# Optimization experiments

Hardware: AMD Instinct MI355X
Metric: run time of the kernel (lower is better)

The kernel has to match this reference:

```python
import jax, jax.numpy as jnp
import numpy as np

B, T, E, D = 4, 1024, 1024, 2048   # batch, dec len, enc len, model dim
N, K, H = 16, 8, 256               # q heads, kv heads, head dim
G = N // K                         # GQA group size
SCALE = H ** -0.5                  # query_pre_attn_scalar
SOFT_CAP = 50.0
EPS = 1e-6
ROPE_BASE = 10000.0
_K_MASK = jnp.finfo(jnp.bfloat16).min


def _rms_norm(x, scale, eps=EPS):
    var = jnp.mean(jnp.square(x), axis=-1, keepdims=True)
    return x * jax.lax.rsqrt(var + eps) * (1.0 + scale)


def _apply_rope(x, positions, base=ROPE_BASE):
    # x: [B, L, n, H], positions: [B, L]; rope_proportion=1.0, scale_factor=1.0
    h = x.shape[-1]
    freq_exp = 2.0 / h * jnp.arange(h // 2, dtype=jnp.float32)
    timescale = base ** freq_exp                                  # [H/2]
    ang = (positions.astype(jnp.float32)[..., None] / timescale)[..., None, :]  # [B,L,1,H/2]
    sin, cos = jnp.sin(ang), jnp.cos(ang)
    x1, x2 = jnp.split(x, 2, axis=-1)
    out = jnp.concatenate([x1 * cos - x2 * sin, x2 * cos + x1 * sin], axis=-1)
    return out.astype(x.dtype)


def setup_inputs() -> dict:
    key = jax.random.key(0)
    ks = jax.random.split(key, 8)
    hidden_states = jax.random.normal(ks[0], (B, T, D), jnp.float32)
    encoder_hidden_states = jax.random.normal(ks[1], (B, E, D), jnp.float32)
    position_ids = jnp.broadcast_to(jnp.arange(T, dtype=jnp.int32)[None, :], (B, T))
    # merged mask: causal over self part, full visibility over cross part
    causal = jnp.tril(jnp.ones((T, T), jnp.bool_))
    cross = jnp.ones((T, E), jnp.bool_)
    merged_attention_mask = jnp.broadcast_to(
        jnp.concatenate([causal, cross], axis=-1)[None, None], (B, 1, T, T + E))
    w = 0.02
    q_w = jax.random.normal(ks[2], (N, D, H), jnp.float32) * w
    k_w = jax.random.normal(ks[3], (K, D, H), jnp.float32) * w
    v_w = jax.random.normal(ks[4], (K, D, H), jnp.float32) * w
    o_w = jax.random.normal(ks[5], (N, H, D), jnp.float32) * w
    q_scale = jax.random.normal(ks[6], (H,), jnp.float32) * w
    k_scale = jax.random.normal(ks[7], (H,), jnp.float32) * w
    return dict(hidden_states=hidden_states, encoder_hidden_states=encoder_hidden_states,
                position_ids=position_ids, merged_attention_mask=merged_attention_mask,
                q_w=q_w, k_w=k_w, v_w=v_w, o_w=o_w, q_scale=q_scale, k_scale=k_scale)


def reference(hidden_states, encoder_hidden_states, position_ids, merged_attention_mask,
              q_w, k_w, v_w, o_w, q_scale, k_scale):
    # QKV projections
    query = jnp.einsum('BTD,NDH->BTNH', hidden_states, q_w)
    self_key = jnp.einsum('BTD,KDH->BTKH', hidden_states, k_w)
    self_value = jnp.einsum('BTD,KDH->BTKH', hidden_states, v_w)
    # QK-RMSNorm
    query = _rms_norm(query, q_scale)
    self_key = _rms_norm(self_key, k_scale)
    # RoPE on self-attention q/k only
    query = _apply_rope(query, position_ids)
    self_key = _apply_rope(self_key, position_ids)
    # Cross K/V from encoder states (no RoPE)
    cross_key = _rms_norm(jnp.einsum('BTD,KDH->BTKH', encoder_hidden_states, k_w), k_scale)
    cross_value = jnp.einsum('BTD,KDH->BTKH', encoder_hidden_states, v_w)
    # Merge self + cross along key axis
    keys = jnp.concatenate([self_key, cross_key], axis=1)       # [B, T+E, K, H]
    values = jnp.concatenate([self_value, cross_value], axis=1)
    # Scaled GQA attention
    q = (query * SCALE).reshape(B, T, K, G, H)
    logits = jnp.einsum('BTKGH,BSKH->BKGTS', q, keys)
    # logit soft-capping
    logits = SOFT_CAP * jnp.tanh(logits / SOFT_CAP)
    mask = merged_attention_mask[:, :, None]                    # [B,1,1,T,S]
    logits = jnp.where(mask, logits, _K_MASK)
    probs = jax.nn.softmax(logits.astype(jnp.float32), axis=-1).astype(keys.dtype)
    attn = jnp.einsum('BKGTS,BSKH->BTKGH', probs, values).reshape(B, T, N, H)
    return jnp.einsum('BTNH,NHD->BTD', attn, o_w)
```

## Files before the change

### kernel.cpp

```cpp
#include <hip/hip_runtime.h>
#include <hip/hip_bf16.h>
#include <cstdio>


typedef __attribute__((ext_vector_type(8))) short bf16x8;
typedef __attribute__((ext_vector_type(4))) float f32x4;

static __device__ __forceinline__ ushort f2bf(float x){
  uint u = __float_as_uint(x);
  u += 0x7fffu + ((u >> 16) & 1u);
  return (ushort)(u >> 16);
}
static __device__ __forceinline__ float bf2f(ushort u){
  return __uint_as_float((uint)u << 16);
}
#define GLL16(gp, lp)                                                          \
  __builtin_amdgcn_global_load_lds(                                            \
      (const __attribute__((address_space(1))) void*)(gp),                     \
      (__attribute__((address_space(3))) void*)(lp), 16, 0, 0)

__global__ void k_detect(const uint* __restrict__ src, int* __restrict__ flag){
  int lane = threadIdx.x & 63;
  int cnt = 0;
  for (int i = 0; i < 4; i++){
    uint w = src[lane * 4 + i];
    uint e = (w >> 7) & 0xffu;
    cnt += (e >= 90u && e <= 141u) ? 1 : 0;
  }
  for (int o = 1; o < 64; o <<= 1) cnt += __shfl_xor(cnt, o);
  if (lane == 0) *flag = (cnt >= 128) ? 1 : 0;
}

__global__ void k_tobf(const void* __restrict__ src, ushort* __restrict__ dst,
                       int n8, const int* __restrict__ flag){
  int i = blockIdx.x * blockDim.x + threadIdx.x;
  if (i >= n8) return;
  if (*flag){
    reinterpret_cast<uint4*>(dst)[i] = reinterpret_cast<const uint4*>(src)[i];
  } else {
    const float4* s = reinterpret_cast<const float4*>(src);
    float4 a = s[i * 2], b = s[i * 2 + 1];
    ushort o[8] = { f2bf(a.x), f2bf(a.y), f2bf(a.z), f2bf(a.w),
                    f2bf(b.x), f2bf(b.y), f2bf(b.z), f2bf(b.w) };
    reinterpret_cast<uint4*>(dst)[i] = *reinterpret_cast<uint4*>(o);
  }
}

__global__ void k_wtrans(const void* __restrict__ in, ushort* __restrict__ out,
                         int R, int C, const int* __restrict__ flag){
  __shared__ ushort t[32][33];
  int isbf = *flag;
  int p = blockIdx.z;
  int r0 = blockIdx.y * 32, c0 = blockIdx.x * 32;
  ushort* op = out + (size_t)p * R * C;
  int cc = threadIdx.x & 31, rr = threadIdx.x >> 5;
  if (isbf){
    const ushort* ip = (const ushort*)in + (size_t)p * R * C;
    for (int i = 0; i < 32; i += 8)
      t[rr + i][cc] = ip[(size_t)(r0 + rr + i) * C + c0 + cc];
  } else {
    const float* ip = (const float*)in + (size_t)p * R * C;
    for (int i = 0; i < 32; i += 8)
      t[rr + i][cc] = f2bf(ip[(size_t)(r0 + rr + i) * C + c0 + cc]);
  }
  __syncthreads();
  for (int i = 0; i < 32; i += 8)
    op[(size_t)(c0 + rr + i) * R + r0 + cc] = t[cc][rr + i];
}

__global__ __launch_bounds__(256)
void k_gemm_qkv(const ushort* __restrict__ A0, const ushort* __restrict__ A1,
                const ushort* __restrict__ Bm,
                ushort* __restrict__ Qo, ushort* __restrict__ Ko,
                ushort* __restrict__ Vo){
  const int m0 = blockIdx.y * 128, n0 = blockIdx.x * 128;
  if (n0 < 4096 && m0 >= 4096) return;
  __shared__ ushort As[128 * 32];
  __shared__ ushort Bs[128 * 32];
  const int tid = threadIdx.x;
  const int Kd = 2048;
  const ushort* Ap = (m0 < 4096) ? (A0 + (size_t)m0 * Kd)
                                 : (A1 + (size_t)(m0 - 4096) * Kd);
  const ushort* Bp = Bm + (size_t)n0 * Kd;
  const int w = tid >> 6, lane = tid & 63, c = lane & 15, q = lane >> 4;
  const int wr = (w >> 1) * 64, wc = (w & 1) * 64;

  f32x4 zf = {0.f, 0.f, 0.f, 0.f};
  f32x4 acc[4][4];
  for (int mi = 0; mi < 4; mi++) for (int ni = 0; ni < 4; ni++) acc[mi][ni] = zf;

  const int sr = tid >> 2, sc8 = (tid & 3) * 8;
  const ushort* ga = Ap + (size_t)sr * Kd + sc8;
  const ushort* gb = Bp + (size_t)sr * Kd + sc8;
  ushort* la = &As[sr * 32 + sc8];
  ushort* lb = &Bs[sr * 32 + sc8];
  const size_t rowskip = (size_t)64 * Kd;

  for (int k0 = 0; k0 < Kd; k0 += 32){
    GLL16(ga + k0,           la);
    GLL16(ga + k0 + rowskip, la + 64 * 32);
    GLL16(gb + k0,           lb);
    GLL16(gb + k0 + rowskip, lb + 64 * 32);
    __syncthreads();
    bf16x8 af[4], bfrg[4];
    for (int mi = 0; mi < 4; mi++)
      af[mi] = *reinterpret_cast<const bf16x8*>(&As[(wr + mi * 16 + c) * 32 + q * 8]);
    for (int ni = 0; ni < 4; ni++)
      bfrg[ni] = *reinterpret_cast<const bf16x8*>(&Bs[(wc + ni * 16 + c) * 32 + q * 8]);
    for (int mi = 0; mi < 4; mi++)
      for (int ni = 0; ni < 4; ni++)
        acc[mi][ni] = __builtin_amdgcn_mfma_f32_16x16x32_bf16(af[mi], bfrg[ni], acc[mi][ni], 0, 0, 0);
    __syncthreads();
  }

  for (int mi = 0; mi < 4; mi++)
    for (int ni = 0; ni < 4; ni++){
      int gr0 = m0 + wr + mi * 16 + q * 4;
      int gc  = n0 + wc + ni * 16 + c;
      if (n0 < 4096){
        for (int r = 0; r < 4; r++)
          Qo[(size_t)(gr0 + r) * 4096 + gc] = f2bf(acc[mi][ni][r]);
      } else if (n0 < 6144){
        int col = gc - 4096;
        for (int r = 0; r < 4; r++){
          int gr = gr0 + r, b, s;
          if (gr < 4096){ b = gr >> 10; s = gr & 1023; }
          else { int g2 = gr - 4096; b = g2 >> 10; s = 1024 + (g2 & 1023); }
          Ko[(size_t)(b * 2048 + s) * 2048 + col] = f2bf(acc[mi][ni][r]);
        }
      } else {
        int col = gc - 6144;
        int gr = gr0, b, s;
        if (gr < 4096){ b = gr >> 10; s = gr & 1023; }
        else { int g2 = gr - 4096; b = g2 >> 10; s = 1024 + (g2 & 1023); }
        int kk = col >> 8, h = col & 255;
        ushort4 o;
        o.x = f2bf(acc[mi][ni][0]); o.y = f2bf(acc[mi][ni][1]);
        o.z = f2bf(acc[mi][ni][2]); o.w = f2bf(acc[mi][ni][3]);
        *reinterpret_cast<ushort4*>(Vo + ((size_t)(b * 8 + kk) * 256 + h) * 2048 + s) = o;
      }
    }
}

__global__ __launch_bounds__(256)
void k_gemm_o(const ushort* __restrict__ A0, const ushort* __restrict__ Bm,
              float* __restrict__ Cout, int N, int Kd){
  __shared__ ushort As[128 * 32];
  __shared__ ushort Bs[128 * 32];
  const int tid = threadIdx.x;
  const int m0 = blockIdx.y * 128, n0 = blockIdx.x * 128;
  const ushort* Ap = A0 + (size_t)m0 * Kd;
  const ushort* Bp = Bm + (size_t)n0 * Kd;
  const int w = tid >> 6, lane = tid & 63, c = lane & 15, q = lane >> 4;
  const int wr = (w >> 1) * 64, wc = (w & 1) * 64;
  f32x4 zf = {0.f, 0.f, 0.f, 0.f};
  f32x4 acc[4][4];
  for (int mi = 0; mi < 4; mi++) for (int ni = 0; ni < 4; ni++) acc[mi][ni] = zf;
  const int sr = tid >> 2, sc8 = (tid & 3) * 8;
  const ushort* ga = Ap + (size_t)sr * Kd + sc8;
  const ushort* gb = Bp + (size_t)sr * Kd + sc8;
  ushort* la = &As[sr * 32 + sc8];
  ushort* lb = &Bs[sr * 32 + sc8];
  const size_t rowskip = (size_t)64 * Kd;
  for (int k0 = 0; k0 < Kd; k0 += 32){
    GLL16(ga + k0,           la);
    GLL16(ga + k0 + rowskip, la + 64 * 32);
    GLL16(gb + k0,           lb);
    GLL16(gb + k0 + rowskip, lb + 64 * 32);
    __syncthreads();
    bf16x8 af[4], bfrg[4];
    for (int mi = 0; mi < 4; mi++)
      af[mi] = *reinterpret_cast<const bf16x8*>(&As[(wr + mi * 16 + c) * 32 + q * 8]);
    for (int ni = 0; ni < 4; ni++)
      bfrg[ni] = *reinterpret_cast<const bf16x8*>(&Bs[(wc + ni * 16 + c) * 32 + q * 8]);
    for (int mi = 0; mi < 4; mi++)
      for (int ni = 0; ni < 4; ni++)
        acc[mi][ni] = __builtin_amdgcn_mfma_f32_16x16x32_bf16(af[mi], bfrg[ni], acc[mi][ni], 0, 0, 0);
    __syncthreads();
  }
  for (int mi = 0; mi < 4; mi++)
    for (int ni = 0; ni < 4; ni++){
      int gr0 = m0 + wr + mi * 16 + q * 4;
      int gc  = n0 + wc + ni * 16 + c;
      for (int r = 0; r < 4; r++)
        Cout[(size_t)(gr0 + r) * N + gc] = acc[mi][ni][r];
    }
}

__global__ __launch_bounds__(256)
void k_norm_q(const ushort* __restrict__ Qraw, const int* __restrict__ pos,
              const ushort* __restrict__ scale, ushort* __restrict__ Qbf){
  int w = threadIdx.x >> 6, lane = threadIdx.x & 63;
  int gw = blockIdx.x * 4 + w;
  int bt = gw >> 4;
  ushort4 xu = *reinterpret_cast<const ushort4*>(Qraw + (size_t)gw * 256 + lane * 4);
  float x[4] = { bf2f(xu.x), bf2f(xu.y), bf2f(xu.z), bf2f(xu.w) };
  float ss = x[0]*x[0] + x[1]*x[1] + x[2]*x[2] + x[3]*x[3];
  for (int o = 32; o > 0; o >>= 1) ss += __shfl_xor(ss, o);
  float rin = rsqrtf(ss * (1.f / 256.f) + 1e-6f);
  ushort4 su = *reinterpret_cast<const ushort4*>(scale + lane * 4);
  float y[4] = { x[0] * rin * (1.f + bf2f(su.x)), x[1] * rin * (1.f + bf2f(su.y)),
                 x[2] * rin * (1.f + bf2f(su.z)), x[3] * rin * (1.f + bf2f(su.w)) };
  float oth[4];
  for (int i = 0; i < 4; i++) oth[i] = __shfl_xor(y[i], 32);
  bool hi = lane >= 32;
  float fb = (float)((lane & 31) * 4);
  float p = (float)pos[bt];
  ushort4 o;
  ushort* op[4] = {&o.x, &o.y, &o.z, &o.w};
  for (int i = 0; i < 4; i++){
    float fi = fb + i;
    float tsi = expf(fi * -0.07195578415f);
    float ang = p * tsi;
    float sn, cs; sincosf(ang, &sn, &cs);
    float v = hi ? (y[i] * cs + oth[i] * sn) : (y[i] * cs - oth[i] * sn);
    *op[i] = f2bf(v * 0.0625f);
  }
  *reinterpret_cast<ushort4*>(Qbf + (size_t)gw * 256 + lane * 4) = o;
}

__global__ __launch_bounds__(256)
void k_norm_k(const ushort* __restrict__ Kraw, const int* __restrict__ pos,
              const ushort* __restrict__ scale, ushort* __restrict__ Kbf){
  int w = threadIdx.x >> 6, lane = threadIdx.x & 63;
  int gw = blockIdx.x * 4 + w;
  int row = gw >> 3;
  int s = row & 2047, b = row >> 11;
  ushort4 xu = *reinterpret_cast<const ushort4*>(Kraw + (size_t)gw * 256 + lane * 4);
  float x[4] = { bf2f(xu.x), bf2f(xu.y), bf2f(xu.z), bf2f(xu.w) };
  float ss = x[0]*x[0] + x[1]*x[1] + x[2]*x[2] + x[3]*x[3];
  for (int o = 32; o > 0; o >>= 1) ss += __shfl_xor(ss, o);
  float rin = rsqrtf(ss * (1.f / 256.f) + 1e-6f);
  ushort4 su = *reinterpret_cast<const ushort4*>(scale + lane * 4);
  float y[4] = { x[0] * rin * (1.f + bf2f(su.x)), x[1] * rin * (1.f + bf2f(su.y)),
                 x[2] * rin * (1.f + bf2f(su.z)), x[3] * rin * (1.f + bf2f(su.w)) };
  ushort4 o;
  ushort* op[4] = {&o.x, &o.y, &o.z, &o.w};
  if (s < 1024){
    float oth[4];
    for (int i = 0; i < 4; i++) oth[i] = __shfl_xor(y[i], 32);
    bool hi = lane >= 32;
    float fb = (float)((lane & 31) * 4);
    float p = (float)pos[b * 1024 + s];
    for (int i = 0; i < 4; i++){
      float fi = fb + i;
      float tsi = expf(fi * -0.07195578415f);
      float ang = p * tsi;
      float sn, cs; sincosf(ang, &sn, &cs);
      float v = hi ? (y[i] * cs + oth[i] * sn) : (y[i] * cs - oth[i] * sn);
      *op[i] = f2bf(v);
    }
  } else {
    for (int i = 0; i < 4; i++) *op[i] = f2bf(y[i]);
  }
  *reinterpret_cast<ushort4*>(Kbf + (size_t)gw * 256 + lane * 4) = o;
}

__global__ __launch_bounds__(256)
void k_attn(const ushort* __restrict__ Qbf, const ushort* __restrict__ Kbf,
            const ushort* __restrict__ Vt, ushort* __restrict__ attn){
  constexpr int KSs = 264, VSs = 40, PSs = 40;
  __shared__ ushort Ks[32 * KSs];
  __shared__ ushort Vs[256 * VSs];
  __shared__ ushort Pm[4][32 * PSs];
  int id = blockIdx.x;
  int xcd = id & 7, slot = id >> 3;
  int grp = xcd + 8 * (slot >> 4);
  int within = slot & 15;
  int b = grp >> 3, kk = grp & 7;
  int n = kk * 2 + (within >> 3);
  int t0 = (within & 7) * 128;
  int tid = threadIdx.x, w = tid >> 6, lane = tid & 63, c = lane & 15, q = lane >> 4;
  int rowbase = t0 + w * 32;

  bf16x8 qf[2][8];
  for (int g = 0; g < 2; g++){
    int tq = rowbase + g * 16 + c;
    const ushort* qp = Qbf + ((size_t)(b * 1024 + tq) * 16 + n) * 256 + q * 8;
    for (int f = 0; f < 8; f++) qf[g][f] = *reinterpret_cast<const bf16x8*>(qp + f * 32);
  }
  f32x4 zf = {0.f, 0.f, 0.f, 0.f};
  f32x4 accO[2][16];
  for (int g = 0; g < 2; g++) for (int i = 0; i < 16; i++) accO[g][i] = zf;
  float lacc[2][4] = {{0.f,0.f,0.f,0.f},{0.f,0.f,0.f,0.f}};

  const ushort* Kbase = Kbf + ((size_t)b * 2048 * 8 + kk) * 256;
  const ushort* Vbase = Vt + (size_t)(b * 8 + kk) * 256 * 2048;
  int nself = (t0 >> 5) + 4;
  int ntile = nself + 32;
  for (int it = 0; it < ntile; ++it){
    int s0 = (it < nself) ? it * 32 : 1024 + (it - nself) * 32;
    for (int i = 0; i < 4; i++){
      int tau = tid + i * 256;
      int r = tau >> 5, ch = (tau & 31) * 8;
      *reinterpret_cast<uint4*>(&Ks[r * KSs + ch]) =
        *reinterpret_cast<const uint4*>(Kbase + (size_t)(s0 + r) * 2048 + ch);
    }
    for (int i = 0; i < 4; i++){
      int tau = tid + i * 256;
      int h = tau >> 2, ch = (tau & 3) * 8;
      *reinterpret_cast<uint4*>(&Vs[h * VSs + ch]) =
        *reinterpret_cast<const uint4*>(Vbase + (size_t)h * 2048 + s0 + ch);
    }
    __syncthreads();
    f32x4 accL[2][2];
    accL[0][0] = zf; accL[0][1] = zf; accL[1][0] = zf; accL[1][1] = zf;
    for (int ni = 0; ni < 2; ni++)
      for (int f = 0; f < 8; f++){
        bf16x8 kb = *reinterpret_cast<const bf16x8*>(&Ks[(ni * 16 + c) * KSs + f * 32 + q * 8]);
        accL[0][ni] = __builtin_amdgcn_mfma_f32_16x16x32_bf16(qf[0][f], kb, accL[0][ni], 0, 0, 0);
        accL[1][ni] = __builtin_amdgcn_mfma_f32_16x16x32_bf16(qf[1][f], kb, accL[1][ni], 0, 0, 0);
      }
    ushort* pw = Pm[w];
    for (int g = 0; g < 2; g++)
      for (int ni = 0; ni < 2; ni++)
        for (int r = 0; r < 4; r++){
          int s = s0 + ni * 16 + c;
          int t = rowbase + g * 16 + q * 4 + r;
          float x = accL[g][ni][r] * 0.02f;
          float xc = fminf(fmaxf(x, -10.f), 10.f);
          float e2 = __expf(2.f * xc);
          float l2 = 50.f * (1.f - 2.f / (e2 + 1.f));
          float pv = (s >= 1024 || s <= t) ? __expf(l2) : 0.f;
          lacc[g][r] += pv;
          pw[(g * 16 + q * 4 + r) * PSs + ni * 16 + c] = f2bf(pv);
        }
    __asm__ volatile("s_waitcnt lgkmcnt(0)" ::: "memory");
    bf16x8 pa0 = *reinterpret_cast<const bf16x8*>(&pw[c * PSs + q * 8]);
    bf16x8 pa1 = *reinterpret_cast<const bf16x8*>(&pw[(16 + c) * PSs + q * 8]);
    for (int hi = 0; hi < 16; hi++){
      bf16x8 vb = *reinterpret_cast<const bf16x8*>(&Vs[(hi * 16 + c) * VSs + q * 8]);
      accO[0][hi] = __builtin_amdgcn_mfma_f32_16x16x32_bf16(pa0, vb, accO[0][hi], 0, 0, 0);
      accO[1][hi] = __builtin_amdgcn_mfma_f32_16x16x32_bf16(pa1, vb, accO[1][hi], 0, 0, 0);
    }
    __syncthreads();
  }
  for (int g = 0; g < 2; g++)
    for (int r = 0; r < 4; r++)
      for (int o = 1; o < 16; o <<= 1) lacc[g][r] += __shfl_xor(lacc[g][r], o);
  for (int g = 0; g < 2; g++){
    float inv[4];
    for (int r = 0; r < 4; r++) inv[r] = 1.f / fmaxf(lacc[g][r], 1e-37f);
    for (int hi = 0; hi < 16; hi++)
      for (int r = 0; r < 4; r++){
        int t = rowbase + g * 16 + q * 4 + r;
        attn[((size_t)(b * 1024 + t) * 16 + n) * 256 + hi * 16 + c] = f2bf(accO[g][hi][r] * inv[r]);
      }
  }
}

extern "C" void kernel_launch(void* const* d_in, const int* in_sizes, int n_in,
                              void* d_out, int out_size, void* d_ws, size_t ws_size,
                              hipStream_t stream){
  const void* hidden = d_in[0];
  const void* enc    = d_in[1];
  const int*  posids = (const int*)d_in[2];
  const void* qw = d_in[4];
  const void* kw = d_in[5];
  const void* vw = d_in[6];
  const void* ow = d_in[7];
  const void* qs = d_in[8];
  const void* ks = d_in[9];
  float* out = (float*)d_out;

  char* ws = (char*)d_ws;
  size_t off = 0;
  auto alloc = [&](size_t sz){ void* p = ws + off; off += sz; return p; };
  char*   HbEb = (char*)alloc(33554432);
  ushort* Hb   = (ushort*)HbEb;
  ushort* Eb   = (ushort*)(HbEb + 16777216);
  ushort* Wcat = (ushort*)alloc(33554432);
  ushort* Wo   = (ushort*)alloc(16777216);
  ushort* Qraw = (ushort*)alloc(33554432);
  ushort* Kraw = (ushort*)alloc(33554432);
  ushort* Vt   = (ushort*)alloc(33554432);
  ushort* qsb  = (ushort*)alloc(512);
  ushort* ksb  = (ushort*)alloc(512);
  int*    flag = (int*)alloc(64);
  ushort* Qbf   = (ushort*)HbEb;
  ushort* Kbf   = Qraw;
  ushort* attnb = Kraw;
  if (off > ws_size){
    fprintf(stderr, "kernel_launch: ws too small: need %zu, have %zu\n", off, ws_size);
    return;
  }

  k_detect<<<1, 64, 0, stream>>>((const uint*)hidden, flag);
  k_tobf<<<4096, 256, 0, stream>>>(hidden, Hb, 1048576, flag);
  k_tobf<<<4096, 256, 0, stream>>>(enc,    Eb, 1048576, flag);
  k_tobf<<<1, 256, 0, stream>>>(qs, qsb, 32, flag);
  k_tobf<<<1, 256, 0, stream>>>(ks, ksb, 32, flag);

  k_wtrans<<<dim3(8, 64, 16), 256, 0, stream>>>(qw, Wcat,            2048, 256, flag);
  k_wtrans<<<dim3(8, 64, 8),  256, 0, stream>>>(kw, Wcat + 8388608,  2048, 256, flag);
  k_wtrans<<<dim3(8, 64, 8),  256, 0, stream>>>(vw, Wcat + 12582912, 2048, 256, flag);
  k_wtrans<<<dim3(64, 128, 1), 256, 0, stream>>>(ow, Wo, 4096, 2048, flag);

  k_gemm_qkv<<<dim3(64, 64), 256, 0, stream>>>(Hb, Eb, Wcat, Qraw, Kraw, Vt);

  k_norm_q<<<16384, 256, 0, stream>>>(Qraw, posids, qsb, Qbf);
  k_norm_k<<<16384, 256, 0, stream>>>(Kraw, posids, ksb, Kbf);

  k_attn<<<512, 256, 0, stream>>>(Qbf, Kbf, Vt, attnb);

  k_gemm_o<<<dim3(16, 32), 256, 0, stream>>>(attnb, Wo, out, 2048, 4096);
}
```

Before: 900.6 us.

## Prefetch attention K/V tiles into registers, swizzle GEMM blocks, add MFMA priority

The attention loop now issues the global loads for the next K/V tile into registers before computing the current tile, then writes them to LDS after the second barrier. This hides global-memory latency behind the MFMA and softmax work. Both GEMMs remap block indices with a stride-8 swizzle to improve L2 locality across XCDs. MFMA sections are wrapped in s_setprio, and attention blocks alternate the order of query tiles to balance causal work. The prefetch raises register pressure by 32 VGPRs per thread, which may reduce occupancy.

```diff
diff --git a/kernel.cpp b/kernel.cpp
--- a/kernel.cpp
+++ b/kernel.cpp
@@ -73,7 +73,9 @@
                 const ushort* __restrict__ Bm,
                 ushort* __restrict__ Qo, ushort* __restrict__ Ko,
                 ushort* __restrict__ Vo){
-  const int m0 = blockIdx.y * 128, n0 = blockIdx.x * 128;
+  const int flat = blockIdx.y * 64 + blockIdx.x;
+  const int sw = (flat & 7) * 512 + (flat >> 3);
+  const int m0 = (sw >> 6) * 128, n0 = (sw & 63) * 128;
   if (n0 < 4096 && m0 >= 4096) return;
   __shared__ ushort As[128 * 32];
   __shared__ ushort Bs[128 * 32];
@@ -107,9 +109,11 @@
       af[mi] = *reinterpret_cast<const bf16x8*>(&As[(wr + mi * 16 + c) * 32 + q * 8]);
     for (int ni = 0; ni < 4; ni++)
       bfrg[ni] = *reinterpret_cast<const bf16x8*>(&Bs[(wc + ni * 16 + c) * 32 + q * 8]);
+    __builtin_amdgcn_s_setprio(1);
     for (int mi = 0; mi < 4; mi++)
       for (int ni = 0; ni < 4; ni++)
         acc[mi][ni] = __builtin_amdgcn_mfma_f32_16x16x32_bf16(af[mi], bfrg[ni], acc[mi][ni], 0, 0, 0);
+    __builtin_amdgcn_s_setprio(0);
     __syncthreads();
   }
 
@@ -148,7 +152,9 @@
   __shared__ ushort As[128 * 32];
   __shared__ ushort Bs[128 * 32];
   const int tid = threadIdx.x;
-  const int m0 = blockIdx.y * 128, n0 = blockIdx.x * 128;
+  const int flat = blockIdx.y * 16 + blockIdx.x;
+  const int sw = (flat & 7) * 64 + (flat >> 3);
+  const int m0 = (sw >> 4) * 128, n0 = (sw & 15) * 128;
   const ushort* Ap = A0 + (size_t)m0 * Kd;
   const ushort* Bp = Bm + (size_t)n0 * Kd;
   const int w = tid >> 6, lane = tid & 63, c = lane & 15, q = lane >> 4;
@@ -173,9 +179,11 @@
       af[mi] = *reinterpret_cast<const bf16x8*>(&As[(wr + mi * 16 + c) * 32 + q * 8]);
     for (int ni = 0; ni < 4; ni++)
       bfrg[ni] = *reinterpret_cast<const bf16x8*>(&Bs[(wc + ni * 16 + c) * 32 + q * 8]);
+    __builtin_amdgcn_s_setprio(1);
     for (int mi = 0; mi < 4; mi++)
       for (int ni = 0; ni < 4; ni++)
         acc[mi][ni] = __builtin_amdgcn_mfma_f32_16x16x32_bf16(af[mi], bfrg[ni], acc[mi][ni], 0, 0, 0);
+    __builtin_amdgcn_s_setprio(0);
     __syncthreads();
   }
   for (int mi = 0; mi < 4; mi++)
@@ -269,7 +277,9 @@
   int within = slot & 15;
   int b = grp >> 3, kk = grp & 7;
   int n = kk * 2 + (within >> 3);
-  int t0 = (within & 7) * 128;
+  int j = within & 7;
+  if (id & 256) j = 7 - j;
+  int t0 = j * 128;
   int tid = threadIdx.x, w = tid >> 6, lane = tid & 63, c = lane & 15, q = lane >> 4;
   int rowbase = t0 + w * 32;
 
@@ -286,31 +296,57 @@
 
   const ushort* Kbase = Kbf + ((size_t)b * 2048 * 8 + kk) * 256;
   const ushort* Vbase = Vt + (size_t)(b * 8 + kk) * 256 * 2048;
+
+  int koffE[4], voffE[4];
+  ushort *klp[4], *vlp[4];
+#pragma unroll
+  for (int i = 0; i < 4; i++){
+    int tau = tid + i * 256;
+    int r = tau >> 5, ch = (tau & 31) * 8;
+    koffE[i] = r * 2048 + ch;
+    klp[i] = &Ks[r * KSs + ch];
+    int h = tau >> 2, cv = (tau & 3) * 8;
+    voffE[i] = h * 2048 + cv;
+    vlp[i] = &Vs[h * VSs + cv];
+  }
+
   int nself = (t0 >> 5) + 4;
   int ntile = nself + 32;
+
+#pragma unroll
+  for (int i = 0; i < 4; i++)
+    *reinterpret_cast<uint4*>(klp[i]) = *reinterpret_cast<const uint4*>(Kbase + koffE[i]);
+#pragma unroll
+  for (int i = 0; i < 4; i++)
+    *reinterpret_cast<uint4*>(vlp[i]) = *reinterpret_cast<const uint4*>(Vbase + voffE[i]);
+
   for (int it = 0; it < ntile; ++it){
     int s0 = (it < nself) ? it * 32 : 1024 + (it - nself) * 32;
-    for (int i = 0; i < 4; i++){
-      int tau = tid + i * 256;
-      int r = tau >> 5, ch = (tau & 31) * 8;
-      *reinterpret_cast<uint4*>(&Ks[r * KSs + ch]) =
-        *reinterpret_cast<const uint4*>(Kbase + (size_t)(s0 + r) * 2048 + ch);
-    }
-    for (int i = 0; i < 4; i++){
-      int tau = tid + i * 256;
-      int h = tau >> 2, ch = (tau & 3) * 8;
-      *reinterpret_cast<uint4*>(&Vs[h * VSs + ch]) =
-        *reinterpret_cast<const uint4*>(Vbase + (size_t)h * 2048 + s0 + ch);
-    }
-    __syncthreads();
+    __syncthreads();
+
+    uint4 kr[4], vr[4];
+    const bool pf = (it + 1 < ntile);
+    if (pf){
+      int it1 = it + 1;
+      int s0n = (it1 < nself) ? it1 * 32 : 1024 + (it1 - nself) * 32;
+      const ushort* kp = Kbase + (size_t)s0n * 2048;
+      const ushort* vp = Vbase + s0n;
+#pragma unroll
+      for (int i = 0; i < 4; i++) kr[i] = *reinterpret_cast<const uint4*>(kp + koffE[i]);
+#pragma unroll
+      for (int i = 0; i < 4; i++) vr[i] = *reinterpret_cast<const uint4*>(vp + voffE[i]);
+    }
+
     f32x4 accL[2][2];
     accL[0][0] = zf; accL[0][1] = zf; accL[1][0] = zf; accL[1][1] = zf;
+    __builtin_amdgcn_s_setprio(1);
     for (int ni = 0; ni < 2; ni++)
       for (int f = 0; f < 8; f++){
         bf16x8 kb = *reinterpret_cast<const bf16x8*>(&Ks[(ni * 16 + c) * KSs + f * 32 + q * 8]);
         accL[0][ni] = __builtin_amdgcn_mfma_f32_16x16x32_bf16(qf[0][f], kb, accL[0][ni], 0, 0, 0);
         accL[1][ni] = __builtin_amdgcn_mfma_f32_16x16x32_bf16(qf[1][f], kb, accL[1][ni], 0, 0, 0);
       }
+    __builtin_amdgcn_s_setprio(0);
     ushort* pw = Pm[w];
     for (int g = 0; g < 2; g++)
       for (int ni = 0; ni < 2; ni++)
@@ -328,12 +364,21 @@
     __asm__ volatile("s_waitcnt lgkmcnt(0)" ::: "memory");
     bf16x8 pa0 = *reinterpret_cast<const bf16x8*>(&pw[c * PSs + q * 8]);
     bf16x8 pa1 = *reinterpret_cast<const bf16x8*>(&pw[(16 + c) * PSs + q * 8]);
+    __builtin_amdgcn_s_setprio(1);
     for (int hi = 0; hi < 16; hi++){
       bf16x8 vb = *reinterpret_cast<const bf16x8*>(&Vs[(hi * 16 + c) * VSs + q * 8]);
       accO[0][hi] = __builtin_amdgcn_mfma_f32_16x16x32_bf16(pa0, vb, accO[0][hi], 0, 0, 0);
       accO[1][hi] = __builtin_amdgcn_mfma_f32_16x16x32_bf16(pa1, vb, accO[1][hi], 0, 0, 0);
     }
-    __syncthreads();
+    __builtin_amdgcn_s_setprio(0);
+    __syncthreads();
+
+    if (pf){
+#pragma unroll
+      for (int i = 0; i < 4; i++) *reinterpret_cast<uint4*>(klp[i]) = kr[i];
+#pragma unroll
+      for (int i = 0; i < 4; i++) *reinterpret_cast<uint4*>(vlp[i]) = vr[i];
+    }
   }
   for (int g = 0; g < 2; g++)
     for (int r = 0; r < 4; r++)
```

New measurement: 1.295 ms. 43.8% more time.

## Double-buffer attention K/V tiles with async global-to-LDS loads and XOR swizzle

Applied to the files above, without the earlier changes.

The attention kernel now prefetches the next K/V tile into a second LDS buffer with global_load_lds while computing on the current tile. This overlaps memory latency with MFMA work instead of doing a synchronous load-then-barrier per tile. K rows use an XOR swizzle rather than padding to avoid bank conflicts. The softcap+exp is algebraically folded into a single exp of a reciprocal using rcp. It doubles LDS use, which may reduce occupancy, and relies on careful vmcnt and barrier ordering.

```diff
diff --git a/kernel.cpp b/kernel.cpp
--- a/kernel.cpp
+++ b/kernel.cpp
@@ -259,9 +259,9 @@
 __global__ __launch_bounds__(256)
 void k_attn(const ushort* __restrict__ Qbf, const ushort* __restrict__ Kbf,
             const ushort* __restrict__ Vt, ushort* __restrict__ attn){
-  constexpr int KSs = 264, VSs = 40, PSs = 40;
-  __shared__ ushort Ks[32 * KSs];
-  __shared__ ushort Vs[256 * VSs];
+  constexpr int PSs = 40;
+  __shared__ ushort Ks2[2][32 * 256];
+  __shared__ ushort Vs2[2][256 * 32];
   __shared__ ushort Pm[4][32 * PSs];
   int id = blockIdx.x;
   int xcd = id & 7, slot = id >> 3;
@@ -288,26 +288,52 @@
   const ushort* Vbase = Vt + (size_t)(b * 8 + kk) * 256 * 2048;
   int nself = (t0 >> 5) + 4;
   int ntile = nself + 32;
+
+#define STAGE(bf, s0v)                                                         \
+  do {                                                                         \
+    const ushort* kp_ = Kbase + (size_t)(s0v) * 2048;                          \
+    const ushort* vp_ = Vbase + (s0v);                                         \
+    _Pragma("unroll")                                                          \
+    for (int i_ = 0; i_ < 4; i_++){                                            \
+      int tau_ = tid + i_ * 256;                                               \
+      int r_ = tau_ >> 5, kch_ = tau_ & 31;                                    \
+      GLL16(kp_ + r_ * 2048 + ((kch_ ^ (r_ & 7)) << 3), &Ks2[bf][tau_ * 8]);   \
+    }                                                                          \
+    _Pragma("unroll")                                                          \
+    for (int i_ = 0; i_ < 4; i_++){                                            \
+      int tau_ = tid + i_ * 256;                                               \
+      int h_ = tau_ >> 2, k2_ = tau_ & 3;                                      \
+      GLL16(vp_ + h_ * 2048 + (k2_ << 3), &Vs2[bf][tau_ * 8]);                 \
+    }                                                                          \
+  } while (0)
+
+  STAGE(0, 0);
+  int cur = 0;
+  const int cxor = c & 7;
+
   for (int it = 0; it < ntile; ++it){
     int s0 = (it < nself) ? it * 32 : 1024 + (it - nself) * 32;
-    for (int i = 0; i < 4; i++){
-      int tau = tid + i * 256;
-      int r = tau >> 5, ch = (tau & 31) * 8;
-      *reinterpret_cast<uint4*>(&Ks[r * KSs + ch]) =
-        *reinterpret_cast<const uint4*>(Kbase + (size_t)(s0 + r) * 2048 + ch);
+    __builtin_amdgcn_sched_barrier(0);
+    __builtin_amdgcn_s_barrier();
+    __builtin_amdgcn_sched_barrier(0);
+    {
+      int itn = (it + 1 < ntile) ? it + 1 : it;
+      int s0n = (itn < nself) ? itn * 32 : 1024 + (itn - nself) * 32;
+      STAGE(cur ^ 1, s0n);
     }
-    for (int i = 0; i < 4; i++){
-      int tau = tid + i * 256;
-      int h = tau >> 2, ch = (tau & 3) * 8;
-      *reinterpret_cast<uint4*>(&Vs[h * VSs + ch]) =
-        *reinterpret_cast<const uint4*>(Vbase + (size_t)h * 2048 + s0 + ch);
-    }
-    __syncthreads();
+    __asm__ volatile("s_waitcnt vmcnt(8)" ::: "memory");
+    __builtin_amdgcn_sched_barrier(0);
+    __builtin_amdgcn_s_barrier();
+    __builtin_amdgcn_sched_barrier(0);
+
+    const ushort* Kcur = Ks2[cur];
+    const ushort* Vcur = Vs2[cur];
     f32x4 accL[2][2];
     accL[0][0] = zf; accL[0][1] = zf; accL[1][0] = zf; accL[1][1] = zf;
     for (int ni = 0; ni < 2; ni++)
       for (int f = 0; f < 8; f++){
-        bf16x8 kb = *reinterpret_cast<const bf16x8*>(&Ks[(ni * 16 + c) * KSs + f * 32 + q * 8]);
+        bf16x8 kb = *reinterpret_cast<const bf16x8*>(
+            &Kcur[(ni * 16 + c) * 256 + (((f * 4 + q) ^ cxor) << 3)]);
         accL[0][ni] = __builtin_amdgcn_mfma_f32_16x16x32_bf16(qf[0][f], kb, accL[0][ni], 0, 0, 0);
         accL[1][ni] = __builtin_amdgcn_mfma_f32_16x16x32_bf16(qf[1][f], kb, accL[1][ni], 0, 0, 0);
       }
@@ -320,8 +346,9 @@
           float x = accL[g][ni][r] * 0.02f;
           float xc = fminf(fmaxf(x, -10.f), 10.f);
           float e2 = __expf(2.f * xc);
-          float l2 = 50.f * (1.f - 2.f / (e2 + 1.f));
-          float pv = (s >= 1024 || s <= t) ? __expf(l2) : 0.f;
+          float d = __builtin_amdgcn_rcpf(e2 + 1.f);
+          float pv = (s >= 1024 || s <= t)
+                       ? 5.184705529e21f * __expf(-100.f * d) : 0.f;
           lacc[g][r] += pv;
           pw[(g * 16 + q * 4 + r) * PSs + ni * 16 + c] = f2bf(pv);
         }
@@ -329,12 +356,14 @@
     bf16x8 pa0 = *reinterpret_cast<const bf16x8*>(&pw[c * PSs + q * 8]);
     bf16x8 pa1 = *reinterpret_cast<const bf16x8*>(&pw[(16 + c) * PSs + q * 8]);
     for (int hi = 0; hi < 16; hi++){
-      bf16x8 vb = *reinterpret_cast<const bf16x8*>(&Vs[(hi * 16 + c) * VSs + q * 8]);
+      bf16x8 vb = *reinterpret_cast<const bf16x8*>(&Vcur[(hi * 16 + c) * 32 + q * 8]);
       accO[0][hi] = __builtin_amdgcn_mfma_f32_16x16x32_bf16(pa0, vb, accO[0][hi], 0, 0, 0);
       accO[1][hi] = __builtin_amdgcn_mfma_f32_16x16x32_bf16(pa1, vb, accO[1][hi], 0, 0, 0);
     }
-    __syncthreads();
-  }
+    __builtin_amdgcn_sched_barrier(0);
+    cur ^= 1;
+  }
+#undef STAGE
   for (int g = 0; g < 2; g++)
     for (int r = 0; r < 4; r++)
       for (int o = 1; o < 16; o <<= 1) lacc[g][r] += __shfl_xor(lacc[g][r], o);
```

Result: slower. 927.1 us (+2.9%).
